# Kernel tuning notes

Hardware: AMD Instinct MI355X
Metric: run time of the kernel (lower is better)

## Reference

```python
import jax, jax.numpy as jnp
import numpy as np

WIN = 8        # window_size
HEADS = 8      # n_heads
SHIFT = WIN // 2

# relative position index (static buffer, n_dim=2)
_coords = np.stack(np.meshgrid(np.arange(WIN), np.arange(WIN), indexing='ij'), 0).reshape(2, WIN * WIN)
_rel = _coords[:, :, None] - _coords[:, None, :] + (WIN - 1)          # [2, w*w, w*w]
REL_IDX = _rel[0] * (2 * WIN - 1) + _rel[1]                            # [w*w, w*w] int


def setup_inputs() -> dict:
    key = jax.random.key(0)
    ks = jax.random.split(key, 6)
    B, C, H, W = 4, 256, 128, 128
    x = jax.random.normal(ks[0], (B, C, H, W), dtype=jnp.float32)
    w_qkv = jax.random.normal(ks[1], (C, 3 * C), dtype=jnp.float32) * 0.02
    b_qkv = jax.random.normal(ks[2], (3 * C,), dtype=jnp.float32) * 0.02
    w_out = jax.random.normal(ks[3], (C, C), dtype=jnp.float32) * 0.02
    b_out = jax.random.normal(ks[4], (C,), dtype=jnp.float32) * 0.02
    bias_table = jax.random.normal(ks[5], ((2 * WIN - 1) ** 2, HEADS), dtype=jnp.float32) * 0.02
    return {"x": x, "w_qkv": w_qkv, "b_qkv": b_qkv, "w_out": w_out, "b_out": b_out, "bias_table": bias_table}


def reference(x, w_qkv, b_qkv, w_out, b_out, bias_table):
    B, C, H, W = x.shape
    w = WIN
    ch = C // HEADS
    xf = jnp.moveaxis(x, 1, -1)                                # [B,H,W,C]
    xf = jnp.roll(xf, (-SHIFT, -SHIFT), axis=(1, 2))           # shifted windows (cyclic)
    # H,W chosen divisible by window_size -> no circular padding needed
    qkv = xf @ w_qkv + b_qkv                                   # [B,H,W,3C]
    Hw, Ww = H // w, W // w
    # contiguous window partition -> [B, nWin, w*w, 3, heads, ch]
    qkv = qkv.reshape(B, Hw, w, Ww, w, 3 * C).transpose(0, 1, 3, 2, 4, 5)
    qkv = qkv.reshape(B, Hw * Ww, w * w, 3, HEADS, ch)
    q = jnp.moveaxis(qkv[..., 0, :, :], -2, 2)                 # [B,nWin,heads,seq,ch]
    k = jnp.moveaxis(qkv[..., 1, :, :], -2, 2)
    v = jnp.moveaxis(qkv[..., 2, :, :], -2, 2)
    bias = bias_table[REL_IDX]                                 # [seq,seq,heads]
    bias = jnp.transpose(bias, (2, 0, 1))                      # [heads,seq,seq]
    scale = 1.0 / jnp.sqrt(jnp.asarray(ch, dtype=q.dtype))
    scores = jnp.einsum('bnhsc,bnhtc->bnhst', q, k) * scale + bias
    attn = jax.nn.softmax(scores, axis=-1)
    out = jnp.einsum('bnhst,bnhtc->bnhsc', attn, v)            # [B,nWin,heads,seq,ch]
    out = jnp.moveaxis(out, 2, -2).reshape(B, Hw, Ww, w, w, C) # merge heads
    out = out.transpose(0, 1, 3, 2, 4, 5).reshape(B, H, W, C)  # un-window
    out = jnp.roll(out, (SHIFT, SHIFT), axis=(1, 2))           # undo shift
    out = out @ w_out + b_out                                  # [B,H,W,Cout]
    return jnp.moveaxis(out, -1, 1)                            # [B,Cout,H,W]
```

## Files before the change

### kernel.cpp

```cpp
#include <hip/hip_runtime.h>

typedef float  f32x4  __attribute__((ext_vector_type(4)));
typedef __bf16 bf16x8 __attribute__((ext_vector_type(8)));
typedef __bf16 bf16x2 __attribute__((ext_vector_type(2)));
typedef short  s16x8  __attribute__((ext_vector_type(8)));
typedef unsigned u32x4 __attribute__((ext_vector_type(4)));

static __device__ __forceinline__ unsigned short f2bf(float f) {
  unsigned u = __builtin_bit_cast(unsigned, f);
  u += 0x7FFFu + ((u >> 16) & 1u);
  return (unsigned short)(u >> 16);
}

static __device__ __forceinline__ unsigned pk2(float a, float b) {
  bf16x2 v = { (__bf16)a, (__bf16)b };
  return __builtin_bit_cast(unsigned, v);
}

static __device__ __forceinline__ f32x4 mfma16(s16x8 a, s16x8 b, f32x4 c) {
  return __builtin_amdgcn_mfma_f32_16x16x32_bf16(
      __builtin_bit_cast(bf16x8, a), __builtin_bit_cast(bf16x8, b), c, 0, 0, 0);
}

static __device__ __forceinline__ void gll16(const void* g, void* lds) {
  __builtin_amdgcn_global_load_lds(
      (const __attribute__((address_space(1))) unsigned int*)g,
      (__attribute__((address_space(3))) unsigned int*)lds, 16, 0, 0);
}

__global__ __launch_bounds__(256) void k_conv_x(const float* __restrict__ x,
                                                unsigned short* __restrict__ xb) {
  __shared__ __align__(16) unsigned short L[512 * 40];
  int bid = blockIdx.x;
  int cchunk = bid & 7, h2 = (bid >> 3) & 1, wy = (bid >> 4) & 15, b = bid >> 8;
  int t = threadIdx.x;
  int cpair = t >> 7, slot = t & 127, lr = slot >> 5, lp = slot & 31;
  int y = (wy * 8 + h2 * 4 + lr + 4) & 127;
  const float* row0 = x + ((size_t)b << 22) + (y << 7);
  int cbase = cchunk * 32;

  for (int it = 0; it < 8; ++it) {
    int cL0 = it * 4 + cpair * 2;
    const float* pa = row0 + ((size_t)(cbase + cL0) << 14) + lp * 4;
    f32x4 a  = *reinterpret_cast<const f32x4*>(pa);
    f32x4 c4 = *reinterpret_cast<const f32x4*>(pa + 16384);
#pragma unroll
    for (int i = 0; i < 4; ++i) {
      int xc = lp * 4 + i;
      int xp = (xc - 4) & 127;
      int wx = xp >> 3, ix = xp & 7;
      int sg = lr * 128 + ix * 16 + wx;
      unsigned pk = (unsigned)f2bf(a[i]) | ((unsigned)f2bf(c4[i]) << 16);
      *reinterpret_cast<unsigned*>(&L[sg * 40 + cL0]) = pk;
    }
  }
  __syncthreads();

  size_t M0 = ((size_t)((b * 16 + wy) * 16)) * 64 + h2 * 32;
  for (int pass = 0; pass < 8; ++pass) {
    int tk = pass * 64 + (t >> 2), p = t & 3;
    int wx = tk >> 5, lr2 = (tk >> 3) & 3, ix = tk & 7;
    int sg = lr2 * 128 + ix * 16 + wx;
    uint4 v = *reinterpret_cast<const uint4*>(&L[sg * 40 + p * 8]);
    size_t m = M0 + (size_t)wx * 64 + lr2 * 8 + ix;
    *reinterpret_cast<uint4*>(&xb[m * 256 + cbase + p * 8]) = v;
  }
}

__global__ __launch_bounds__(256) void k_conv_w(const float* __restrict__ wqkv,
                                                const float* __restrict__ wout,
                                                unsigned short* __restrict__ wqkvT,
                                                unsigned short* __restrict__ woutT) {
  int j = blockIdx.x, c = threadIdx.x;
  if (j < 768) wqkvT[j * 256 + c] = f2bf(wqkv[c * 768 + j]);
  else { int jj = j - 768; woutT[jj * 256 + c] = f2bf(wout[c * 256 + jj]); }
}

__global__ __launch_bounds__(256) void k_bias(const float* __restrict__ btab,
                                              float* __restrict__ bmat) {
  int i = blockIdx.x * 256 + threadIdx.x;
  int t = i & 63, s = (i >> 6) & 63, h = i >> 12;
  int idx = ((s >> 3) - (t >> 3) + 7) * 15 + ((s & 7) - (t & 7) + 7);
  bmat[i] = btab[idx * 8 + h];
}

__global__ __launch_bounds__(256, 4) void k_qkvattn(const unsigned short* __restrict__ xb,
                                                    const unsigned short* __restrict__ wT,
                                                    const float* __restrict__ bqkv,
                                                    const float* __restrict__ bmat,
                                                    unsigned short* __restrict__ ao) {
  __shared__ __align__(16) unsigned char smA[32768];
  int lane = threadIdx.x & 63, w = threadIdx.x >> 6;
  int bid = blockIdx.x;
  int sb = (bid & 7) * 256 + (bid >> 3);
  int win = sb >> 1, h = (sb & 1) * 4 + w;
  int g = lane >> 4, l15 = lane & 15;
  int m0 = win * 64;
  const float scale = 0.17677669529663687f;

#pragma unroll
  for (int i = 0; i < 8; ++i) {
    int inst = w * 8 + i;
    int row = inst * 2 + (lane >> 5);
    int sg = (lane & 31) ^ (row & 7);
    gll16(xb + (size_t)(m0 + row) * 256 + sg * 8, smA + inst * 1024);
  }
  __syncthreads();

  const unsigned short* Wq = wT + (size_t)(h * 32 + l15) * 256 + g * 8;
  const unsigned short* Wk = Wq + 65536;
  const unsigned short* Wv = Wk + 65536;

  f32x4 aQ[2][4], aK[2][4];
#pragma unroll
  for (int jt = 0; jt < 2; ++jt)
#pragma unroll
    for (int mt = 0; mt < 4; ++mt) {
      aQ[jt][mt] = f32x4{0.f, 0.f, 0.f, 0.f};
      aK[jt][mt] = f32x4{0.f, 0.f, 0.f, 0.f};
    }
#pragma unroll
  for (int ks = 0; ks < 8; ++ks) {
    int off = ks * 32;
    s16x8 fq[2], fk[2];
#pragma unroll
    for (int jt = 0; jt < 2; ++jt) {
      fq[jt] = *reinterpret_cast<const s16x8*>(Wq + (size_t)jt * 4096 + off);
      fk[jt] = *reinterpret_cast<const s16x8*>(Wk + (size_t)jt * 4096 + off);
    }
    s16x8 af[4];
#pragma unroll
    for (int mt = 0; mt < 4; ++mt) {
      int row = mt * 16 + l15;
      int chunk = (ks * 4 + g) ^ (row & 7);
      af[mt] = *reinterpret_cast<const s16x8*>(smA + row * 512 + chunk * 16);
    }
    __builtin_amdgcn_s_setprio(1);
#pragma unroll
    for (int jt = 0; jt < 2; ++jt)
#pragma unroll
      for (int mt = 0; mt < 4; ++mt) {
        aQ[jt][mt] = mfma16(fq[jt], af[mt], aQ[jt][mt]);
        aK[jt][mt] = mfma16(fk[jt], af[mt], aK[jt][mt]);
      }
    __builtin_amdgcn_s_setprio(0);
  }

  f32x4 bq2[2], bk2[2];
#pragma unroll
  for (int jt = 0; jt < 2; ++jt) {
    bq2[jt] = *reinterpret_cast<const f32x4*>(&bqkv[h * 32 + jt * 16 + g * 4]);
    bk2[jt] = *reinterpret_cast<const f32x4*>(&bqkv[256 + h * 32 + jt * 16 + g * 4]);
  }
  s16x8 kfr[4], qfr[4];
#pragma unroll
  for (int ti = 0; ti < 4; ++ti) {
    u32x4 uk, uq;
    uk[0] = pk2(aK[0][ti][0] + bk2[0][0], aK[0][ti][1] + bk2[0][1]);
    uk[1] = pk2(aK[0][ti][2] + bk2[0][2], aK[0][ti][3] + bk2[0][3]);
    uk[2] = pk2(aK[1][ti][0] + bk2[1][0], aK[1][ti][1] + bk2[1][1]);
    uk[3] = pk2(aK[1][ti][2] + bk2[1][2], aK[1][ti][3] + bk2[1][3]);
    kfr[ti] = __builtin_bit_cast(s16x8, uk);
    uq[0] = pk2((aQ[0][ti][0] + bq2[0][0]) * scale, (aQ[0][ti][1] + bq2[0][1]) * scale);
    uq[1] = pk2((aQ[0][ti][2] + bq2[0][2]) * scale, (aQ[0][ti][3] + bq2[0][3]) * scale);
    uq[2] = pk2((aQ[1][ti][0] + bq2[1][0]) * scale, (aQ[1][ti][1] + bq2[1][1]) * scale);
    uq[3] = pk2((aQ[1][ti][2] + bq2[1][2]) * scale, (aQ[1][ti][3] + bq2[1][3]) * scale);
    qfr[ti] = __builtin_bit_cast(s16x8, uq);
  }

  f32x4 aV[4][2];
#pragma unroll
  for (int mt = 0; mt < 4; ++mt)
#pragma unroll
    for (int ni = 0; ni < 2; ++ni) aV[mt][ni] = f32x4{0.f, 0.f, 0.f, 0.f};
#pragma unroll
  for (int ks = 0; ks < 8; ++ks) {
    int off = ks * 32;
    s16x8 fv[2];
#pragma unroll
    for (int jt = 0; jt < 2; ++jt)
      fv[jt] = *reinterpret_cast<const s16x8*>(Wv + (size_t)jt * 4096 + off);
    s16x8 af[4];
#pragma unroll
    for (int mt = 0; mt < 4; ++mt) {
      int row = mt * 16 + l15;
      int chunk = (ks * 4 + g) ^ (row & 7);
      af[mt] = *reinterpret_cast<const s16x8*>(smA + row * 512 + chunk * 16);
    }
    __builtin_amdgcn_s_setprio(1);
#pragma unroll
    for (int mt = 0; mt < 4; ++mt)
#pragma unroll
      for (int ni = 0; ni < 2; ++ni)
        aV[mt][ni] = mfma16(af[mt], fv[ni], aV[mt][ni]);
    __builtin_amdgcn_s_setprio(0);
  }

  float bv2[2];
  bv2[0] = bqkv[512 + h * 32 + l15];
  bv2[1] = bqkv[512 + h * 32 + 16 + l15];
  s16x8 vfr[2][2];
#pragma unroll
  for (int ni = 0; ni < 2; ++ni)
#pragma unroll
    for (int ks = 0; ks < 2; ++ks) {
      u32x4 uv;
      uv[0] = pk2(aV[2 * ks][ni][0] + bv2[ni], aV[2 * ks][ni][1] + bv2[ni]);
      uv[1] = pk2(aV[2 * ks][ni][2] + bv2[ni], aV[2 * ks][ni][3] + bv2[ni]);
      uv[2] = pk2(aV[2 * ks + 1][ni][0] + bv2[ni], aV[2 * ks + 1][ni][1] + bv2[ni]);
      uv[3] = pk2(aV[2 * ks + 1][ni][2] + bv2[ni], aV[2 * ks + 1][ni][3] + bv2[ni]);
      vfr[ni][ks] = __builtin_bit_cast(s16x8, uv);
    }

  const float* bm = bmat + (h << 12);
  f32x4 ot[2][4];
#pragma unroll
  for (int ni = 0; ni < 2; ++ni)
#pragma unroll
    for (int mi = 0; mi < 4; ++mi) ot[ni][mi] = f32x4{0.f, 0.f, 0.f, 0.f};

  float m01[4], s01[4], inv[4];

  {
    f32x4 sth[2][4];
    __builtin_amdgcn_s_setprio(1);
#pragma unroll
    for (int th = 0; th < 2; ++th)
#pragma unroll
      for (int si = 0; si < 4; ++si)
        sth[th][si] = mfma16(kfr[th], qfr[si], f32x4{0.f, 0.f, 0.f, 0.f});
    __builtin_amdgcn_s_setprio(0);
#pragma unroll
    for (int si = 0; si < 4; ++si) {
      int srow = (si * 16 + l15) * 64;
      f32x4 v0 = sth[0][si] + *reinterpret_cast<const f32x4*>(&bm[srow + g * 4]);
      f32x4 v1 = sth[1][si] + *reinterpret_cast<const f32x4*>(&bm[srow + 16 + g * 4]);
      float mx = fmaxf(fmaxf(fmaxf(v0[0], v0[1]), fmaxf(v0[2], v0[3])),
                       fmaxf(fmaxf(v1[0], v1[1]), fmaxf(v1[2], v1[3])));
      mx = fmaxf(mx, __shfl_xor(mx, 16));
      mx = fmaxf(mx, __shfl_xor(mx, 32));
      f32x4 p0, p1;
      float sum = 0.f;
#pragma unroll
      for (int r = 0; r < 4; ++r) { p0[r] = __expf(v0[r] - mx); sum += p0[r]; }
#pragma unroll
      for (int r = 0; r < 4; ++r) { p1[r] = __expf(v1[r] - mx); sum += p1[r]; }
      sum += __shfl_xor(sum, 16);
      sum += __shfl_xor(sum, 32);
      m01[si] = mx; s01[si] = sum;
      u32x4 up;
      up[0] = pk2(p0[0], p0[1]); up[1] = pk2(p0[2], p0[3]);
      up[2] = pk2(p1[0], p1[1]); up[3] = pk2(p1[2], p1[3]);
      s16x8 pf = __builtin_bit_cast(s16x8, up);
      ot[0][si] = mfma16(vfr[0][0], pf, ot[0][si]);
      ot[1][si] = mfma16(vfr[1][0], pf, ot[1][si]);
    }
  }

  {
    f32x4 sth[2][4];
    __builtin_amdgcn_s_setprio(1);
#pragma unroll
    for (int th = 0; th < 2; ++th)
#pragma unroll
      for (int si = 0; si < 4; ++si)
        sth[th][si] = mfma16(kfr[2 + th], qfr[si], f32x4{0.f, 0.f, 0.f, 0.f});
    __builtin_amdgcn_s_setprio(0);
#pragma unroll
    for (int si = 0; si < 4; ++si) {
      int srow = (si * 16 + l15) * 64;
      f32x4 v0 = sth[0][si] + *reinterpret_cast<const f32x4*>(&bm[srow + 32 + g * 4]);
      f32x4 v1 = sth[1][si] + *reinterpret_cast<const f32x4*>(&bm[srow + 48 + g * 4]);
      float m23 = fmaxf(fmaxf(fmaxf(v0[0], v0[1]), fmaxf(v0[2], v0[3])),
                        fmaxf(fmaxf(v1[0], v1[1]), fmaxf(v1[2], v1[3])));
      m23 = fmaxf(m23, __shfl_xor(m23, 16));
      m23 = fmaxf(m23, __shfl_xor(m23, 32));
      float m = fmaxf(m01[si], m23);
      float c01 = __expf(m01[si] - m);
      f32x4 p0, p1;
      float sum = 0.f;
#pragma unroll
      for (int r = 0; r < 4; ++r) { p0[r] = __expf(v0[r] - m); sum += p0[r]; }
#pragma unroll
      for (int r = 0; r < 4; ++r) { p1[r] = __expf(v1[r] - m); sum += p1[r]; }
      sum += __shfl_xor(sum, 16);
      sum += __shfl_xor(sum, 32);
      inv[si] = 1.0f / (c01 * s01[si] + sum);
      u32x4 up;
      up[0] = pk2(p0[0], p0[1]); up[1] = pk2(p0[2], p0[3]);
      up[2] = pk2(p1[0], p1[1]); up[3] = pk2(p1[2], p1[3]);
      s16x8 pf = __builtin_bit_cast(s16x8, up);
      ot[0][si] *= c01;
      ot[1][si] *= c01;
      ot[0][si] = mfma16(vfr[0][1], pf, ot[0][si]);
      ot[1][si] = mfma16(vfr[1][1], pf, ot[1][si]);
    }
  }

#pragma unroll
  for (int ni = 0; ni < 2; ++ni)
#pragma unroll
    for (int mi = 0; mi < 4; ++mi) {
      float iv = inv[mi];
      uint2 pk;
      pk.x = pk2(ot[ni][mi][0] * iv, ot[ni][mi][1] * iv);
      pk.y = pk2(ot[ni][mi][2] * iv, ot[ni][mi][3] * iv);
      size_t m = (size_t)(win * 64 + mi * 16 + l15);
      *reinterpret_cast<uint2*>(&ao[m * 256 + h * 32 + ni * 16 + g * 4]) = pk;
    }
}

__global__ __launch_bounds__(256) void k_oproj(const unsigned short* __restrict__ ao,
                                               const unsigned short* __restrict__ wT,
                                               const float* __restrict__ bout,
                                               float* __restrict__ out) {
  __shared__ __align__(16) unsigned short Al[128 * 64];
  __shared__ __align__(16) unsigned short Bl[128 * 64];
  int j0 = blockIdx.x * 128, m0 = blockIdx.y * 128;
  int lane = threadIdx.x & 63, w = threadIdx.x >> 6;
  int wm = w >> 1, wn = w & 1, g = lane >> 4, l15 = lane & 15;

  f32x4 acc[4][4];
#pragma unroll
  for (int i = 0; i < 4; ++i)
#pragma unroll
    for (int j = 0; j < 4; ++j) acc[i][j] = f32x4{0.f, 0.f, 0.f, 0.f};

  for (int kt = 0; kt < 4; ++kt) {
    int k0 = kt * 64;
#pragma unroll
    for (int i = 0; i < 4; ++i) {
      int r0 = (w * 4 + i) * 8;
      int row = r0 + (lane >> 3);
      int sg = (lane & 7) ^ (row & 7);
      gll16(ao + (size_t)(m0 + row) * 256 + k0 + sg * 8, &Al[r0 * 64]);
      gll16(wT + (size_t)(j0 + row) * 256 + k0 + sg * 8, &Bl[r0 * 64]);
    }
    __syncthreads();
#pragma unroll
    for (int ks = 0; ks < 2; ++ks) {
      s16x8 af[4], bf[4];
#pragma unroll
      for (int mi = 0; mi < 4; ++mi) {
        int row = wm * 64 + mi * 16 + l15;
        int chunk = (ks * 4 + g) ^ (row & 7);
        af[mi] = *reinterpret_cast<const s16x8*>(&Al[row * 64 + chunk * 8]);
      }
#pragma unroll
      for (int ni = 0; ni < 4; ++ni) {
        int row = wn * 64 + ni * 16 + l15;
        int chunk = (ks * 4 + g) ^ (row & 7);
        bf[ni] = *reinterpret_cast<const s16x8*>(&Bl[row * 64 + chunk * 8]);
      }
#pragma unroll
      for (int mi = 0; mi < 4; ++mi)
#pragma unroll
        for (int ni = 0; ni < 4; ++ni)
          acc[mi][ni] = mfma16(af[mi], bf[ni], acc[mi][ni]);
    }
    __syncthreads();
  }

#pragma unroll
  for (int ni = 0; ni < 4; ++ni) {
    int j = j0 + wn * 64 + ni * 16 + l15;
    float bj = bout[j];
#pragma unroll
    for (int mi = 0; mi < 4; ++mi) {
      int mb = m0 + wm * 64 + mi * 16 + g * 4;
      int win = mb >> 6, seq0 = mb & 63;
      int b = win >> 8, wy = (win >> 4) & 15, wx = win & 15;
      int iy = seq0 >> 3, ix0 = seq0 & 7;
      int y = (wy * 8 + iy + 4) & 127;
      int x0 = (wx * 8 + ix0 + 4) & 127;
      f32x4 v = acc[mi][ni];
      v.x += bj; v.y += bj; v.z += bj; v.w += bj;
      *reinterpret_cast<f32x4*>(&out[(((size_t)b * 256 + j) << 14) + (y << 7) + x0]) = v;
    }
  }
}

extern "C" void kernel_launch(void* const* d_in, const int* in_sizes, int n_in,
                              void* d_out, int out_size, void* d_ws, size_t ws_size,
                              hipStream_t stream) {
  const float* x    = (const float*)d_in[0];
  const float* wqkv = (const float*)d_in[1];
  const float* bqkv = (const float*)d_in[2];
  const float* wout = (const float*)d_in[3];
  const float* bout = (const float*)d_in[4];
  const float* btab = (const float*)d_in[5];
  float* out = (float*)d_out;
  char* ws = (char*)d_ws;

  unsigned short* XB = (unsigned short*)(ws);
  unsigned short* AO = (unsigned short*)(ws + 33554432);
  unsigned short* WQ = (unsigned short*)(ws + 67108864);
  unsigned short* WO = (unsigned short*)(ws + 67502080);
  float*          BM = (float*)(ws + 67633152);
  if (ws_size < 67764224ull) return;

  k_conv_x<<<1024, 256, 0, stream>>>(x, XB);
  k_conv_w<<<1024, 256, 0, stream>>>(wqkv, wout, WQ, WO);
  k_bias<<<128, 256, 0, stream>>>(btab, BM);
  k_qkvattn<<<2048, 256, 0, stream>>>(XB, WQ, bqkv, BM, AO);
  k_oproj<<<dim3(2, 512), 256, 0, stream>>>(AO, WO, bout, out);
}
```

Before: 135.0 us.

## Fuse output projection into window attention kernel with one block per window

```diff
diff --git a/kernel.cpp b/kernel.cpp
--- a/kernel.cpp
+++ b/kernel.cpp
@@ -84,23 +84,25 @@
   bmat[i] = btab[idx * 8 + h];
 }
 
-__global__ __launch_bounds__(256, 4) void k_qkvattn(const unsigned short* __restrict__ xb,
-                                                    const unsigned short* __restrict__ wT,
-                                                    const float* __restrict__ bqkv,
-                                                    const float* __restrict__ bmat,
-                                                    unsigned short* __restrict__ ao) {
+__global__ __launch_bounds__(512, 4) void k_fused(const unsigned short* __restrict__ xb,
+                                                  const unsigned short* __restrict__ wT,
+                                                  const unsigned short* __restrict__ woT,
+                                                  const float* __restrict__ bqkv,
+                                                  const float* __restrict__ bmat,
+                                                  const float* __restrict__ bout,
+                                                  float* __restrict__ out) {
   __shared__ __align__(16) unsigned char smA[32768];
   int lane = threadIdx.x & 63, w = threadIdx.x >> 6;
   int bid = blockIdx.x;
-  int sb = (bid & 7) * 256 + (bid >> 3);
-  int win = sb >> 1, h = (sb & 1) * 4 + w;
+  int win = (bid & 7) * 128 + (bid >> 3);
+  int h = w;
   int g = lane >> 4, l15 = lane & 15;
   int m0 = win * 64;
   const float scale = 0.17677669529663687f;
 
 #pragma unroll
-  for (int i = 0; i < 8; ++i) {
-    int inst = w * 8 + i;
+  for (int i = 0; i < 4; ++i) {
+    int inst = w * 4 + i;
     int row = inst * 2 + (lane >> 5);
     int sg = (lane & 31) ^ (row & 7);
     gll16(xb + (size_t)(m0 + row) * 256 + sg * 8, smA + inst * 1024);
@@ -217,165 +219,128 @@
 #pragma unroll
   for (int ni = 0; ni < 2; ++ni)
 #pragma unroll
-    for (int mi = 0; mi < 4; ++mi) ot[ni][mi] = f32x4{0.f, 0.f, 0.f, 0.f};
+    for (int si = 0; si < 4; ++si) ot[ni][si] = f32x4{0.f, 0.f, 0.f, 0.f};
 
   float m01[4], s01[4], inv[4];
 
-  {
-    f32x4 sth[2][4];
+#pragma unroll
+  for (int si = 0; si < 4; ++si) {
+    f32x4 s0 = mfma16(kfr[0], qfr[si], f32x4{0.f, 0.f, 0.f, 0.f});
+    f32x4 s1 = mfma16(kfr[1], qfr[si], f32x4{0.f, 0.f, 0.f, 0.f});
+    int srow = (si * 16 + l15) * 64;
+    f32x4 v0 = s0 + *reinterpret_cast<const f32x4*>(&bm[srow + g * 4]);
+    f32x4 v1 = s1 + *reinterpret_cast<const f32x4*>(&bm[srow + 16 + g * 4]);
+    float mx = fmaxf(fmaxf(fmaxf(v0[0], v0[1]), fmaxf(v0[2], v0[3])),
+                     fmaxf(fmaxf(v1[0], v1[1]), fmaxf(v1[2], v1[3])));
+    mx = fmaxf(mx, __shfl_xor(mx, 16));
+    mx = fmaxf(mx, __shfl_xor(mx, 32));
+    f32x4 p0, p1;
+    float sum = 0.f;
+#pragma unroll
+    for (int r = 0; r < 4; ++r) { p0[r] = __expf(v0[r] - mx); sum += p0[r]; }
+#pragma unroll
+    for (int r = 0; r < 4; ++r) { p1[r] = __expf(v1[r] - mx); sum += p1[r]; }
+    sum += __shfl_xor(sum, 16);
+    sum += __shfl_xor(sum, 32);
+    m01[si] = mx; s01[si] = sum;
+    u32x4 up;
+    up[0] = pk2(p0[0], p0[1]); up[1] = pk2(p0[2], p0[3]);
+    up[2] = pk2(p1[0], p1[1]); up[3] = pk2(p1[2], p1[3]);
+    s16x8 pf = __builtin_bit_cast(s16x8, up);
+    ot[0][si] = mfma16(vfr[0][0], pf, ot[0][si]);
+    ot[1][si] = mfma16(vfr[1][0], pf, ot[1][si]);
+  }
+
+#pragma unroll
+  for (int si = 0; si < 4; ++si) {
+    f32x4 s0 = mfma16(kfr[2], qfr[si], f32x4{0.f, 0.f, 0.f, 0.f});
+    f32x4 s1 = mfma16(kfr[3], qfr[si], f32x4{0.f, 0.f, 0.f, 0.f});
+    int srow = (si * 16 + l15) * 64;
+    f32x4 v0 = s0 + *reinterpret_cast<const f32x4*>(&bm[srow + 32 + g * 4]);
+    f32x4 v1 = s1 + *reinterpret_cast<const f32x4*>(&bm[srow + 48 + g * 4]);
+    float m23 = fmaxf(fmaxf(fmaxf(v0[0], v0[1]), fmaxf(v0[2], v0[3])),
+                      fmaxf(fmaxf(v1[0], v1[1]), fmaxf(v1[2], v1[3])));
+    m23 = fmaxf(m23, __shfl_xor(m23, 16));
+    m23 = fmaxf(m23, __shfl_xor(m23, 32));
+    float m = fmaxf(m01[si], m23);
+    float c01 = __expf(m01[si] - m);
+    f32x4 p0, p1;
+    float sum = 0.f;
+#pragma unroll
+    for (int r = 0; r < 4; ++r) { p0[r] = __expf(v0[r] - m); sum += p0[r]; }
+#pragma unroll
+    for (int r = 0; r < 4; ++r) { p1[r] = __expf(v1[r] - m); sum += p1[r]; }
+    sum += __shfl_xor(sum, 16);
+    sum += __shfl_xor(sum, 32);
+    inv[si] = 1.0f / (c01 * s01[si] + sum);
+    u32x4 up;
+    up[0] = pk2(p0[0], p0[1]); up[1] = pk2(p0[2], p0[3]);
+    up[2] = pk2(p1[0], p1[1]); up[3] = pk2(p1[2], p1[3]);
+    s16x8 pf = __builtin_bit_cast(s16x8, up);
+    ot[0][si] *= c01;
+    ot[1][si] *= c01;
+    ot[0][si] = mfma16(vfr[0][1], pf, ot[0][si]);
+    ot[1][si] = mfma16(vfr[1][1], pf, ot[1][si]);
+  }
+
+  __syncthreads();
+#pragma unroll
+  for (int ni = 0; ni < 2; ++ni)
+#pragma unroll
+    for (int si = 0; si < 4; ++si) {
+      float iv = inv[si];
+      int s = si * 16 + l15;
+      int c0 = h * 32 + ni * 16 + g * 4;
+      uint2 pk;
+      pk.x = pk2(ot[ni][si][0] * iv, ot[ni][si][1] * iv);
+      pk.y = pk2(ot[ni][si][2] * iv, ot[ni][si][3] * iv);
+      *reinterpret_cast<uint2*>(
+          smA + s * 512 + (((c0 >> 3) ^ (s & 7)) * 16) + (c0 & 7) * 2) = pk;
+    }
+  __syncthreads();
+
+  f32x4 acc[4][2];
+#pragma unroll
+  for (int mt = 0; mt < 4; ++mt)
+#pragma unroll
+    for (int nt = 0; nt < 2; ++nt) acc[mt][nt] = f32x4{0.f, 0.f, 0.f, 0.f};
+#pragma unroll
+  for (int kk = 0; kk < 8; ++kk) {
+    s16x8 bfr[2];
+#pragma unroll
+    for (int nt = 0; nt < 2; ++nt)
+      bfr[nt] = *reinterpret_cast<const s16x8*>(
+          woT + (size_t)(w * 32 + nt * 16 + l15) * 256 + kk * 32 + g * 8);
+    s16x8 af[4];
+#pragma unroll
+    for (int mt = 0; mt < 4; ++mt) {
+      int row = mt * 16 + l15;
+      int chunk = (kk * 4 + g) ^ (row & 7);
+      af[mt] = *reinterpret_cast<const s16x8*>(smA + row * 512 + chunk * 16);
+    }
     __builtin_amdgcn_s_setprio(1);
 #pragma unroll
-    for (int th = 0; th < 2; ++th)
-#pragma unroll
-      for (int si = 0; si < 4; ++si)
-        sth[th][si] = mfma16(kfr[th], qfr[si], f32x4{0.f, 0.f, 0.f, 0.f});
+    for (int mt = 0; mt < 4; ++mt)
+#pragma unroll
+      for (int nt = 0; nt < 2; ++nt)
+        acc[mt][nt] = mfma16(af[mt], bfr[nt], acc[mt][nt]);
     __builtin_amdgcn_s_setprio(0);
-#pragma unroll
-    for (int si = 0; si < 4; ++si) {
-      int srow = (si * 16 + l15) * 64;
-      f32x4 v0 = sth[0][si] + *reinterpret_cast<const f32x4*>(&bm[srow + g * 4]);
-      f32x4 v1 = sth[1][si] + *reinterpret_cast<const f32x4*>(&bm[srow + 16 + g * 4]);
-      float mx = fmaxf(fmaxf(fmaxf(v0[0], v0[1]), fmaxf(v0[2], v0[3])),
-                       fmaxf(fmaxf(v1[0], v1[1]), fmaxf(v1[2], v1[3])));
-      mx = fmaxf(mx, __shfl_xor(mx, 16));
-      mx = fmaxf(mx, __shfl_xor(mx, 32));
-      f32x4 p0, p1;
-      float sum = 0.f;
-#pragma unroll
-      for (int r = 0; r < 4; ++r) { p0[r] = __expf(v0[r] - mx); sum += p0[r]; }
-#pragma unroll
-      for (int r = 0; r < 4; ++r) { p1[r] = __expf(v1[r] - mx); sum += p1[r]; }
-      sum += __shfl_xor(sum, 16);
-      sum += __shfl_xor(sum, 32);
-      m01[si] = mx; s01[si] = sum;
-      u32x4 up;
-      up[0] = pk2(p0[0], p0[1]); up[1] = pk2(p0[2], p0[3]);
-      up[2] = pk2(p1[0], p1[1]); up[3] = pk2(p1[2], p1[3]);
-      s16x8 pf = __builtin_bit_cast(s16x8, up);
-      ot[0][si] = mfma16(vfr[0][0], pf, ot[0][si]);
-      ot[1][si] = mfma16(vfr[1][0], pf, ot[1][si]);
-    }
-  }
-
-  {
-    f32x4 sth[2][4];
-    __builtin_amdgcn_s_setprio(1);
-#pragma unroll
-    for (int th = 0; th < 2; ++th)
-#pragma unroll
-      for (int si = 0; si < 4; ++si)
-        sth[th][si] = mfma16(kfr[2 + th], qfr[si], f32x4{0.f, 0.f, 0.f, 0.f});
-    __builtin_amdgcn_s_setprio(0);
-#pragma unroll
-    for (int si = 0; si < 4; ++si) {
-      int srow = (si * 16 + l15) * 64;
-      f32x4 v0 = sth[0][si] + *reinterpret_cast<const f32x4*>(&bm[srow + 32 + g * 4]);
-      f32x4 v1 = sth[1][si] + *reinterpret_cast<const f32x4*>(&bm[srow + 48 + g * 4]);
-      float m23 = fmaxf(fmaxf(fmaxf(v0[0], v0[1]), fmaxf(v0[2], v0[3])),
-                        fmaxf(fmaxf(v1[0], v1[1]), fmaxf(v1[2], v1[3])));
-      m23 = fmaxf(m23, __shfl_xor(m23, 16));
-      m23 = fmaxf(m23, __shfl_xor(m23, 32));
-      float m = fmaxf(m01[si], m23);
-      float c01 = __expf(m01[si] - m);
-      f32x4 p0, p1;
-      float sum = 0.f;
-#pragma unroll
-      for (int r = 0; r < 4; ++r) { p0[r] = __expf(v0[r] - m); sum += p0[r]; }
-#pragma unroll
-      for (int r = 0; r < 4; ++r) { p1[r] = __expf(v1[r] - m); sum += p1[r]; }
-      sum += __shfl_xor(sum, 16);
-      sum += __shfl_xor(sum, 32);
-      inv[si] = 1.0f / (c01 * s01[si] + sum);
-      u32x4 up;
-      up[0] = pk2(p0[0], p0[1]); up[1] = pk2(p0[2], p0[3]);
-      up[2] = pk2(p1[0], p1[1]); up[3] = pk2(p1[2], p1[3]);
-      s16x8 pf = __builtin_bit_cast(s16x8, up);
-      ot[0][si] *= c01;
-      ot[1][si] *= c01;
-      ot[0][si] = mfma16(vfr[0][1], pf, ot[0][si]);
-      ot[1][si] = mfma16(vfr[1][1], pf, ot[1][si]);
-    }
-  }
-
-#pragma unroll
-  for (int ni = 0; ni < 2; ++ni)
-#pragma unroll
-    for (int mi = 0; mi < 4; ++mi) {
-      float iv = inv[mi];
-      uint2 pk;
-      pk.x = pk2(ot[ni][mi][0] * iv, ot[ni][mi][1] * iv);
-      pk.y = pk2(ot[ni][mi][2] * iv, ot[ni][mi][3] * iv);
-      size_t m = (size_t)(win * 64 + mi * 16 + l15);
-      *reinterpret_cast<uint2*>(&ao[m * 256 + h * 32 + ni * 16 + g * 4]) = pk;
-    }
-}
-
-__global__ __launch_bounds__(256) void k_oproj(const unsigned short* __restrict__ ao,
-                                               const unsigned short* __restrict__ wT,
-                                               const float* __restrict__ bout,
-                                               float* __restrict__ out) {
-  __shared__ __align__(16) unsigned short Al[128 * 64];
-  __shared__ __align__(16) unsigned short Bl[128 * 64];
-  int j0 = blockIdx.x * 128, m0 = blockIdx.y * 128;
-  int lane = threadIdx.x & 63, w = threadIdx.x >> 6;
-  int wm = w >> 1, wn = w & 1, g = lane >> 4, l15 = lane & 15;
-
-  f32x4 acc[4][4];
-#pragma unroll
-  for (int i = 0; i < 4; ++i)
-#pragma unroll
-    for (int j = 0; j < 4; ++j) acc[i][j] = f32x4{0.f, 0.f, 0.f, 0.f};
-
-  for (int kt = 0; kt < 4; ++kt) {
-    int k0 = kt * 64;
-#pragma unroll
-    for (int i = 0; i < 4; ++i) {
-      int r0 = (w * 4 + i) * 8;
-      int row = r0 + (lane >> 3);
-      int sg = (lane & 7) ^ (row & 7);
-      gll16(ao + (size_t)(m0 + row) * 256 + k0 + sg * 8, &Al[r0 * 64]);
-      gll16(wT + (size_t)(j0 + row) * 256 + k0 + sg * 8, &Bl[r0 * 64]);
-    }
-    __syncthreads();
-#pragma unroll
-    for (int ks = 0; ks < 2; ++ks) {
-      s16x8 af[4], bf[4];
-#pragma unroll
-      for (int mi = 0; mi < 4; ++mi) {
-        int row = wm * 64 + mi * 16 + l15;
-        int chunk = (ks * 4 + g) ^ (row & 7);
-        af[mi] = *reinterpret_cast<const s16x8*>(&Al[row * 64 + chunk * 8]);
-      }
-#pragma unroll
-      for (int ni = 0; ni < 4; ++ni) {
-        int row = wn * 64 + ni * 16 + l15;
-        int chunk = (ks * 4 + g) ^ (row & 7);
-        bf[ni] = *reinterpret_cast<const s16x8*>(&Bl[row * 64 + chunk * 8]);
-      }
-#pragma unroll
-      for (int mi = 0; mi < 4; ++mi)
-#pragma unroll
-        for (int ni = 0; ni < 4; ++ni)
-          acc[mi][ni] = mfma16(af[mi], bf[ni], acc[mi][ni]);
-    }
-    __syncthreads();
-  }
-
-#pragma unroll
-  for (int ni = 0; ni < 4; ++ni) {
-    int j = j0 + wn * 64 + ni * 16 + l15;
+  }
+
+  int b = win >> 8, wy = (win >> 4) & 15, wx = win & 15;
+#pragma unroll
+  for (int nt = 0; nt < 2; ++nt) {
+    int j = w * 32 + nt * 16 + l15;
     float bj = bout[j];
 #pragma unroll
-    for (int mi = 0; mi < 4; ++mi) {
-      int mb = m0 + wm * 64 + mi * 16 + g * 4;
-      int win = mb >> 6, seq0 = mb & 63;
-      int b = win >> 8, wy = (win >> 4) & 15, wx = win & 15;
+    for (int mt = 0; mt < 4; ++mt) {
+      int seq0 = mt * 16 + g * 4;
       int iy = seq0 >> 3, ix0 = seq0 & 7;
       int y = (wy * 8 + iy + 4) & 127;
       int x0 = (wx * 8 + ix0 + 4) & 127;
-      f32x4 v = acc[mi][ni];
+      f32x4 v = acc[mt][nt];
       v.x += bj; v.y += bj; v.z += bj; v.w += bj;
-      *reinterpret_cast<f32x4*>(&out[(((size_t)b * 256 + j) << 14) + (y << 7) + x0]) = v;
+      *reinterpret_cast<f32x4*>(&out[(((size_t)(b * 256 + j)) << 14) + (y << 7) + x0]) = v;
     }
   }
 }
@@ -393,15 +358,13 @@
   char* ws = (char*)d_ws;
 
   unsigned short* XB = (unsigned short*)(ws);
-  unsigned short* AO = (unsigned short*)(ws + 33554432);
-  unsigned short* WQ = (unsigned short*)(ws + 67108864);
-  unsigned short* WO = (unsigned short*)(ws + 67502080);
-  float*          BM = (float*)(ws + 67633152);
-  if (ws_size < 67764224ull) return;
+  unsigned short* WQ = (unsigned short*)(ws + 33554432);
+  unsigned short* WO = (unsigned short*)(ws + 33947648);
+  float*          BM = (float*)(ws + 34078720);
+  if (ws_size < 34209792ull) return;
 
   k_conv_x<<<1024, 256, 0, stream>>>(x, XB);
   k_conv_w<<<1024, 256, 0, stream>>>(wqkv, wout, WQ, WO);
   k_bias<<<128, 256, 0, stream>>>(btab, BM);
-  k_qkvattn<<<2048, 256, 0, stream>>>(XB, WQ, bqkv, BM, AO);
-  k_oproj<<<dim3(2, 512), 256, 0, stream>>>(AO, WO, bout, out);
-}
+  k_fused<<<1024, 512, 0, stream>>>(XB, WQ, WO, bqkv, BM, bout, out);
+}
```

Result: faster. 125.7 us (median of 3 runs) (-6.8%).
